# Performance work log

Measured on AMD Instinct MI355X. Metric: run time of the kernel, lower is better.

Reference implementation:

```python
import jax, jax.numpy as jnp
import numpy as np

N = 50000          # num nodes
E = 800000         # num edges
DIN = 128          # in_channels
C = 64             # out_channels per head
H = 2              # heads
ED = 32            # edge_dim


def setup_inputs() -> dict:
    key = jax.random.key(0)
    ks = jax.random.split(key, 12)
    s = 1.0 / np.sqrt(DIN)
    se = 1.0 / np.sqrt(ED)
    return {
        "x": jax.random.normal(ks[0], (N, DIN), dtype=jnp.float32),
        "edge_index": jax.random.randint(ks[1], (2, E), 0, N, dtype=jnp.int32),
        "edge_attr": jax.random.normal(ks[2], (E, ED), dtype=jnp.float32),
        "Wq": jax.random.uniform(ks[3], (DIN, H * C), jnp.float32, -s, s),
        "bq": jax.random.uniform(ks[4], (H * C,), jnp.float32, -s, s),
        "Wk": jax.random.uniform(ks[5], (DIN, H * C), jnp.float32, -s, s),
        "bk": jax.random.uniform(ks[6], (H * C,), jnp.float32, -s, s),
        "Wv": jax.random.uniform(ks[7], (DIN, H * C), jnp.float32, -s, s),
        "bv": jax.random.uniform(ks[8], (H * C,), jnp.float32, -s, s),
        "We": jax.random.uniform(ks[9], (ED, H * C), jnp.float32, -se, se),
        "Wskip": jax.random.uniform(ks[10], (DIN, H * C), jnp.float32, -s, s),
        "bskip": jax.random.uniform(ks[11], (H * C,), jnp.float32, -s, s),
    }


def reference(x, edge_index, edge_attr, Wq, bq, Wk, bk, Wv, bv, We, Wskip, bskip):
    src, dst = edge_index[0], edge_index[1]
    # node-level projections [N, H, C]
    q = (x @ Wq + bq).reshape(N, H, C)
    k = (x @ Wk + bk).reshape(N, H, C)
    v = (x @ Wv + bv).reshape(N, H, C)
    e = (edge_attr @ We).reshape(E, H, C)  # lin_edge, no bias

    # per-edge gather
    q_e = q[dst]              # [E, H, C]
    k_e = k[src] + e          # key gets edge features
    alpha = jnp.einsum("ehc,ehc->eh", q_e, k_e) / jnp.sqrt(jnp.float32(C))

    # segment softmax over incoming edges of each dst node
    m = jax.ops.segment_max(alpha, dst, num_segments=N)       # [N, H]
    alpha = jnp.exp(alpha - m[dst])
    denom = jax.ops.segment_sum(alpha, dst, num_segments=N)   # [N, H]
    alpha = alpha / (denom[dst] + 1e-16)

    # weighted aggregation of values (value also gets edge features)
    msg = (v[src] + e) * alpha[..., None]                     # [E, H, C]
    out = jax.ops.segment_sum(msg, dst, num_segments=N)       # [N, H, C]
    out = out.reshape(N, H * C)

    # root weight skip connection (concat=True, beta=False)
    return out + x @ Wskip + bskip
```

## Files before the change

kernel.cpp:

```cpp
#include <hip/hip_runtime.h>
#include <cstdint>

#define NN 50000
#define EE 800000
#define DINC 128
#define HC 128
#define EDC 32
#define CAP 56
#define TILES 1563
#define SCAT_BLKS 3125
#define NB_SCAN 196
#define PREW_GRID (145 + NB_SCAN)

typedef __attribute__((ext_vector_type(8))) short short8;
typedef __attribute__((ext_vector_type(4))) float floatx4;

__device__ __forceinline__ unsigned int pk2(float a, float b){
  unsigned int ua = __float_as_uint(a), ub = __float_as_uint(b);
  ua = (ua + 0x7FFFu + ((ua >> 16) & 1u)) >> 16;
  ub = (ub + 0x7FFFu + ((ub >> 16) & 1u)) & 0xFFFF0000u;
  return ua | ub;
}
__device__ __forceinline__ float bflo(unsigned int p){ return __uint_as_float(p << 16); }
__device__ __forceinline__ float bfhi(unsigned int p){ return __uint_as_float(p & 0xFFFF0000u); }

__device__ __forceinline__ float red32(float r){
  r += __int_as_float(__builtin_amdgcn_update_dpp(0, __float_as_int(r), 0xB1, 0xF, 0xF, true));
  r += __int_as_float(__builtin_amdgcn_update_dpp(0, __float_as_int(r), 0x4E, 0xF, 0xF, true));
  r += __int_as_float(__builtin_amdgcn_update_dpp(0, __float_as_int(r), 0x141, 0xF, 0xF, true));
  r += __int_as_float(__builtin_amdgcn_update_dpp(0, __float_as_int(r), 0x140, 0xF, 0xF, true));
  r += __shfl_xor(r, 16, 32);
  return r;
}

__global__ __launch_bounds__(256) void k_prew(
    const float* __restrict__ Wq, const float* __restrict__ Wk,
    const float* __restrict__ Wv, const float* __restrict__ Wsk,
    const float* __restrict__ We, const float* __restrict__ bq,
    unsigned int* __restrict__ Wp, unsigned int* __restrict__ Wp5,
    float* __restrict__ Pb, int* __restrict__ cnt)
{
  const int b = blockIdx.x, tid = threadIdx.x;
  if (b < 128){
    int idx = b*256 + tid;
    int mat = idx >> 13;
    int r   = idx & 8191;
    int kp  = r >> 7;
    int n   = r & 127;
    const float* W = (mat==0)?Wq:(mat==1)?Wk:(mat==2)?Wv:Wsk;
    Wp[(mat<<13) + n*64 + kp] = pk2(W[(2*kp)*HC + n], W[(2*kp+1)*HC + n]);
  } else if (b < 144){
    if (!Wp5) return;
    int t = (b-128)*256 + tid;
    int kp = t >> 6, n = t & 63;
    int h = n >> 5, j = n & 31;
    const float* wq0 = Wq + (2*kp)*HC + h*64;
    const float* wq1 = wq0 + HC;
    const float* wer = We + j*HC + h*64;
    float d0 = 0.f, d1 = 0.f;
    #pragma unroll 8
    for (int c = 0; c < 64; ++c){
      float w = wer[c];
      d0 += wq0[c]*w; d1 += wq1[c]*w;
    }
    Wp5[n*64 + kp] = pk2(d0, d1);
  } else if (b == 144){
    if (!Wp5 || tid >= 64) return;
    int n = tid, h = n >> 5, j = n & 31;
    const float* wer = We + j*HC + h*64;
    const float* bqh = bq + h*64;
    float s = 0.f;
    #pragma unroll 8
    for (int c = 0; c < 64; ++c) s += bqh[c]*wer[c];
    Pb[n] = s;
  } else {
    int idx = (b-145)*256 + tid;
    if (idx < NN) cnt[idx] = 0;
  }
}

__global__ __launch_bounds__(256) void k_fused(
    const float* __restrict__ x, const unsigned int* __restrict__ Wp,
    const unsigned int* __restrict__ Wp5, const float* __restrict__ Pb,
    const float* __restrict__ bq, const float* __restrict__ bk,
    const float* __restrict__ bv, const float* __restrict__ bsk,
    const int* __restrict__ ei,
    unsigned int* __restrict__ qbf, unsigned int* __restrict__ kvb,
    float* __restrict__ out, float* __restrict__ Pfl,
    int* __restrict__ cnt, int* __restrict__ eidl,
    const int do_scatter)
{
  __shared__ unsigned int sx[32*68];

  if (do_scatter && blockIdx.x >= TILES){
    int e = (blockIdx.x - TILES)*256 + threadIdx.x;
    if (e < EE){
      int d = ei[EE + e];
      int pos = atomicAdd(cnt + d, 1);
      if (pos < CAP) eidl[d*CAP + pos] = e;
    }
    return;
  }

  const int tid = threadIdx.x;
  const int bm  = blockIdx.x * 32;

  for (int idx = tid; idx < 32*32; idx += 256){
    int row = idx >> 5, kq = idx & 31;
    int gr = bm + row;
    unsigned int p0 = 0u, p1 = 0u;
    if (gr < NN){
      float4 v = *(const float4*)(x + (size_t)gr*DINC + 4*kq);
      p0 = pk2(v.x, v.y); p1 = pk2(v.z, v.w);
    }
    sx[row*68 + 2*kq]     = p0;
    sx[row*68 + 2*kq + 1] = p1;
  }
  __syncthreads();

  const int l = tid & 63, wid = tid >> 6;
  const int lm = l & 15, ks = l >> 4;
  const int pe = lm & 1;
  const int n0 = wid * 32;

  short8 a_f[4][2];
  #pragma unroll
  for (int kb = 0; kb < 4; ++kb){
    a_f[kb][0] = *(const short8*)(sx + lm*68      + kb*16 + ks*4);
    a_f[kb][1] = *(const short8*)(sx + (16+lm)*68 + kb*16 + ks*4);
  }

  #pragma unroll
  for (int mat = 0; mat < 4; ++mat){
    const unsigned int* wp = Wp + (mat<<13);
    const float* bi = (mat==0)?bq:(mat==1)?bk:(mat==2)?bv:bsk;

    floatx4 acc[2][2];
    #pragma unroll
    for (int mt=0;mt<2;mt++)
      #pragma unroll
      for (int nt=0;nt<2;nt++) acc[mt][nt] = (floatx4){0.f,0.f,0.f,0.f};

    #pragma unroll
    for (int kb = 0; kb < 4; ++kb){
      short8 b0 = *(const short8*)(wp + (n0+lm)*64    + kb*16 + ks*4);
      short8 b1 = *(const short8*)(wp + (n0+16+lm)*64 + kb*16 + ks*4);
      acc[0][0] = __builtin_amdgcn_mfma_f32_16x16x32_bf16(a_f[kb][0], b0, acc[0][0], 0, 0, 0);
      acc[0][1] = __builtin_amdgcn_mfma_f32_16x16x32_bf16(a_f[kb][0], b1, acc[0][1], 0, 0, 0);
      acc[1][0] = __builtin_amdgcn_mfma_f32_16x16x32_bf16(a_f[kb][1], b0, acc[1][0], 0, 0, 0);
      acc[1][1] = __builtin_amdgcn_mfma_f32_16x16x32_bf16(a_f[kb][1], b1, acc[1][1], 0, 0, 0);
    }

    if (mat < 3){
      #pragma unroll
      for (int nt=0; nt<2; ++nt){
        const int cbase = n0 + nt*16 + (lm & ~1);
        float2 bb = *(const float2*)(bi + cbase);
        const int cp = cbase >> 1;
        #pragma unroll
        for (int mt=0; mt<2; ++mt){
          #pragma unroll
          for (int s=0; s<2; ++s){
            float a_even = acc[mt][nt][2*s];
            float a_odd  = acc[mt][nt][2*s+1];
            float sw_even = __shfl_xor(a_even, 1, 64);
            float sw_odd  = __shfl_xor(a_odd,  1, 64);
            float self = pe ? a_odd  : a_even;
            float part = pe ? sw_odd : sw_even;
            float lo = pe ? part : self;
            float hi = pe ? self : part;
            unsigned int pv = pk2(lo + bb.x, hi + bb.y);
            int gr = bm + mt*16 + ks*4 + 2*s + pe;
            if (gr < NN){
              if (mat == 0)      qbf[gr*64 + cp] = pv;
              else if (mat == 1) kvb[(size_t)gr*128 + cp]      = pv;
              else               kvb[(size_t)gr*128 + 64 + cp] = pv;
            }
          }
        }
      }
    } else {
      #pragma unroll
      for (int nt=0; nt<2; ++nt){
        const int col = n0 + nt*16 + lm;
        float bs = bi[col];
        #pragma unroll
        for (int mt=0; mt<2; ++mt){
          #pragma unroll
          for (int r=0; r<4; ++r){
            int gr = bm + mt*16 + ks*4 + r;
            if (gr < NN) out[(size_t)gr*HC + col] = acc[mt][nt][r] + bs;
          }
        }
      }
    }
  }

  if (Pfl != nullptr){
    const int mt = wid >> 1;
    const int nq = (wid & 1) * 32;
    floatx4 accp[2];
    accp[0] = (floatx4){0.f,0.f,0.f,0.f};
    accp[1] = (floatx4){0.f,0.f,0.f,0.f};
    #pragma unroll
    for (int kb = 0; kb < 4; ++kb){
      short8 b0 = *(const short8*)(Wp5 + (nq+lm)*64    + kb*16 + ks*4);
      short8 b1 = *(const short8*)(Wp5 + (nq+16+lm)*64 + kb*16 + ks*4);
      accp[0] = __builtin_amdgcn_mfma_f32_16x16x32_bf16(a_f[kb][mt], b0, accp[0], 0, 0, 0);
      accp[1] = __builtin_amdgcn_mfma_f32_16x16x32_bf16(a_f[kb][mt], b1, accp[1], 0, 0, 0);
    }
    #pragma unroll
    for (int nt=0; nt<2; ++nt){
      const int col = nq + nt*16 + lm;
      float bs = Pb[col];
      #pragma unroll
      for (int r=0; r<4; ++r){
        int gr = bm + mt*16 + ks*4 + r;
        if (gr < NN) Pfl[(size_t)gr*64 + col] = accp[nt][r] + bs;
      }
    }
  }
}

__global__ __launch_bounds__(256) void k_count(const int* __restrict__ ei,
    int* __restrict__ cnt)
{
  int e = blockIdx.x*256 + threadIdx.x;
  if (e < EE) atomicAdd(cnt + ei[EE + e], 1);
}
__global__ __launch_bounds__(256) void k_blksum(const int* __restrict__ cnt,
    int* __restrict__ bsum)
{
  __shared__ int s[256];
  int t = threadIdx.x, i = blockIdx.x*256 + t;
  s[t] = (i < NN) ? cnt[i] : 0;
  __syncthreads();
  for (int d = 128; d > 0; d >>= 1){
    if (t < d) s[t] += s[t + d];
    __syncthreads();
  }
  if (t == 0) bsum[blockIdx.x] = s[0];
}
__global__ __launch_bounds__(256) void k_bscan(const int* __restrict__ bsum,
    int* __restrict__ bpre)
{
  __shared__ int s[256];
  int t = threadIdx.x;
  int v = (t < NB_SCAN) ? bsum[t] : 0;
  s[t] = v;
  __syncthreads();
  for (int d = 1; d < 256; d <<= 1){
    int u = (t >= d) ? s[t - d] : 0;
    __syncthreads();
    s[t] += u;
    __syncthreads();
  }
  if (t < NB_SCAN) bpre[t] = s[t] - v;
}
__global__ __launch_bounds__(256) void k_scan3(const int* __restrict__ cnt,
    const int* __restrict__ bpre, int* __restrict__ off, int* __restrict__ woff)
{
  __shared__ int s[256];
  int t = threadIdx.x, i = blockIdx.x*256 + t;
  int v = (i < NN) ? cnt[i] : 0;
  s[t] = v;
  __syncthreads();
  for (int d = 1; d < 256; d <<= 1){
    int u = (t >= d) ? s[t - d] : 0;
    __syncthreads();
    s[t] += u;
    __syncthreads();
  }
  if (i < NN){
    int o = bpre[blockIdx.x] + s[t] - v;
    off[i] = o; woff[i] = o;
  }
}
__global__ __launch_bounds__(256) void k_scatter(const int* __restrict__ ei,
    int* __restrict__ woff, int* __restrict__ eidl)
{
  int e = blockIdx.x*256 + threadIdx.x;
  if (e < EE){
    int d = ei[EE + e];
    int pos = atomicAdd(woff + d, 1);
    eidl[pos] = e;
  }
}

template<int HASP>
__global__ __launch_bounds__(256) void k_agg(
    const float* __restrict__ eattr, const float* __restrict__ We,
    const unsigned int* __restrict__ qbf, const unsigned int* __restrict__ kvb,
    const int* __restrict__ ei,
    const int* __restrict__ cnt, const int* __restrict__ off,
    const int* __restrict__ eidl, const int fixed, const float* __restrict__ Pfl,
    float* __restrict__ out)
{
  __shared__ float sWeT[128*33];
  __shared__ float sWea[256];
  const int tid = threadIdx.x;
  for (int idx = tid; idx < EDC*HC; idx += 256){
    int jj = idx >> 7, col = idx & 127;
    sWeT[col*33 + jj] = We[idx];
  }
  __syncthreads();

  const int wid = tid >> 6, l = tid & 63;
  const int node = blockIdx.x*4 + wid;
  const int h = l >> 5, j = l & 31;

  int deg = cnt[node]; if (deg > CAP) deg = CAP;
  const size_t beg = fixed ? (size_t)node*CAP : (size_t)off[node];
  int eidL = 0, srcL = 0;
  if (deg > 0){
    eidL = eidl[beg + ((l < deg) ? l : 0)];
    srcL = ei[eidL];
  }
  const unsigned int eaOff = (unsigned int)eidL * (EDC*4);
  const unsigned int kOff  = (unsigned int)srcL * 512u;
  const unsigned int jB = (unsigned int)j * 4u;
  const unsigned int lB = (unsigned int)l * 4u;
  const char* eac = (const char*)eattr;
  const char* kvc = (const char*)kvb;

  const float SC = 0.18033688f;
  unsigned int qp = qbf[node*64 + l];
  float q0 = bflo(qp)*SC, q1 = bfhi(qp)*SC;
  float Pl;
  if (HASP){
    Pl = Pfl[(size_t)node*64 + l] * SC;
  } else {
    const uint4* qrow4 = (const uint4*)(qbf + node*64 + h*32);
    const float* wt = sWeT + (h*64)*33 + j;
    float s = 0.f;
    #pragma unroll
    for (int c4 = 0; c4 < 8; ++c4){
      uint4 u = qrow4[c4];
      int b = 8*c4;
      s += bflo(u.x)*wt[(b+0)*33] + bfhi(u.x)*wt[(b+1)*33];
      s += bflo(u.y)*wt[(b+2)*33] + bfhi(u.y)*wt[(b+3)*33];
      s += bflo(u.z)*wt[(b+4)*33] + bfhi(u.z)*wt[(b+5)*33];
      s += bflo(u.w)*wt[(b+6)*33] + bfhi(u.w)*wt[(b+7)*33];
    }
    Pl = s*SC;
  }

#define GATHER(base, EA, KK, VV)                                 \
  {                                                              \
    _Pragma("unroll")                                            \
    for (int t = 0; t < 4; ++t){                                 \
      int s = (base) + t;                                        \
      int it = (s < deg) ? s : 0;                                \
      unsigned int eo = (unsigned int)__shfl((int)eaOff, it, 64) + jB; \
      unsigned int ko = (unsigned int)__shfl((int)kOff,  it, 64) + lB; \
      EA[t] = *(const float*)(eac + eo);                         \
      KK[t] = *(const unsigned int*)(kvc + ko);                  \
      VV[t] = *(const unsigned int*)(kvc + ko + 256);            \
    }                                                            \
  }

  float acc0=0.f, acc1=0.f, wea=0.f, den=0.f;
  if (deg > 0){
    float ea0[4], ea1[4], ea2[4];
    unsigned int kk0[4], kk1[4], kk2[4], vv0[4], vv1[4], vv2[4];
    GATHER(0, ea0, kk0, vv0);
    GATHER(4, ea1, kk1, vv1);
    GATHER(8, ea2, kk2, vv2);

    for (int i = 0; i < deg; i += 4){
      float ean[4]; unsigned int kkn[4], vvn[4];
      if (i + 12 < deg){
        GATHER(i+12, ean, kkn, vvn);
      }
      float p[4];
      #pragma unroll
      for (int t = 0; t < 4; ++t)
        p[t] = q0*bflo(kk0[t]) + q1*bfhi(kk0[t]) + Pl*ea0[t];
      #pragma unroll
      for (int t = 0; t < 4; ++t) p[t] = red32(p[t]);
      const int nb = deg - i;
      #pragma unroll
      for (int t = 0; t < 4; ++t){
        float a = __builtin_amdgcn_exp2f(p[t]);
        if (t > 0) a = (t < nb) ? a : 0.f;
        den  += a;
        acc0 += a*bflo(vv0[t]);
        acc1 += a*bfhi(vv0[t]);
        wea  += a*ea0[t];
      }
      #pragma unroll
      for (int t = 0; t < 4; ++t){
        ea0[t] = ea1[t]; kk0[t] = kk1[t]; vv0[t] = vv1[t];
        ea1[t] = ea2[t]; kk1[t] = kk2[t]; vv1[t] = vv2[t];
        ea2[t] = ean[t]; kk2[t] = kkn[t]; vv2[t] = vvn[t];
      }
    }
  }
#undef GATHER

  sWea[tid] = wea;
  __syncthreads();
  float rden = 1.0f/(den + 1e-16f);
  float e0 = 0.f, e1 = 0.f;
  const float* w0 = sWeT + (2*l)*33;
  const float* w1 = sWeT + (2*l+1)*33;
  const float* wv = sWea + wid*64 + h*32;
  #pragma unroll
  for (int jj = 0; jj < 32; jj += 4){
    float4 w4 = *(const float4*)(wv + jj);
    e0 += w4.x*w0[jj]; e1 += w4.x*w1[jj];
    e0 += w4.y*w0[jj+1]; e1 += w4.y*w1[jj+1];
    e0 += w4.z*w0[jj+2]; e1 += w4.z*w1[jj+2];
    e0 += w4.w*w0[jj+3]; e1 += w4.w*w1[jj+3];
  }
  float2 sk = *(const float2*)(out + (size_t)node*HC + 2*l);
  float2 o;
  o.x = sk.x + (acc0 + e0)*rden;
  o.y = sk.y + (acc1 + e1)*rden;
  *(float2*)(out + (size_t)node*HC + 2*l) = o;
}

extern "C" void kernel_launch(void* const* d_in, const int* in_sizes, int n_in,
                              void* d_out, int out_size, void* d_ws, size_t ws_size,
                              hipStream_t stream)
{
  const float* x   = (const float*)d_in[0];
  const int*   ei  = (const int*)d_in[1];
  const float* ea  = (const float*)d_in[2];
  const float* Wq  = (const float*)d_in[3];
  const float* bq  = (const float*)d_in[4];
  const float* Wk  = (const float*)d_in[5];
  const float* bk  = (const float*)d_in[6];
  const float* Wv  = (const float*)d_in[7];
  const float* bv  = (const float*)d_in[8];
  const float* We  = (const float*)d_in[9];
  const float* Wsk = (const float*)d_in[10];
  const float* bsk = (const float*)d_in[11];
  float* out = (float*)d_out;

  char* ws = (char*)d_ws;
  unsigned int* qbf = (unsigned int*)(ws);
  unsigned int* kvb = (unsigned int*)(ws + 12800000);
  int* cnt = (int*)(ws + 38400000);

  if (ws_size >= 62800000ull){
    int* eidl = (int*)(ws + 38600000);
    unsigned int* Wp  = (unsigned int*)(ws + 49800064);
    unsigned int* Wp5 = (unsigned int*)(ws + 49931264);
    float* Pb  = (float*)(ws + 49947648);
    float* Pfl = (float*)(ws + 49948160);
    k_prew<<<PREW_GRID, 256, 0, stream>>>(Wq, Wk, Wv, Wsk, We, bq, Wp, Wp5, Pb, cnt);
    k_fused<<<TILES + SCAT_BLKS, 256, 0, stream>>>(
        x, Wp, Wp5, Pb, bq, bk, bv, bsk, ei, qbf, kvb, out, Pfl, cnt, eidl, 1);
    k_agg<1><<<12500, 256, 0, stream>>>(ea, We, qbf, kvb, ei,
                                        cnt, (const int*)nullptr, eidl, 1, Pfl, out);
  } else if (ws_size >= 50000000ull){
    int* eidl = (int*)(ws + 38600000);
    unsigned int* Wp = (unsigned int*)(ws + 49800064);
    k_prew<<<PREW_GRID, 256, 0, stream>>>(Wq, Wk, Wv, Wsk, We, bq, Wp, nullptr, nullptr, cnt);
    k_fused<<<TILES + SCAT_BLKS, 256, 0, stream>>>(
        x, Wp, nullptr, nullptr, bq, bk, bv, bsk, ei, qbf, kvb, out, nullptr, cnt, eidl, 1);
    k_agg<0><<<12500, 256, 0, stream>>>(ea, We, qbf, kvb, ei,
                                        cnt, (const int*)nullptr, eidl, 1, nullptr, out);
  } else {
    int* off  = (int*)(ws + 38600000);
    int* woff = (int*)(ws + 38800000);
    int* bsum = (int*)(ws + 39000000);
    int* bpre = (int*)(ws + 39001024);
    int* eidl = (int*)(ws + 39002048);
    unsigned int* Wp = (unsigned int*)(ws + 42202112);
    k_prew<<<PREW_GRID, 256, 0, stream>>>(Wq, Wk, Wv, Wsk, We, bq, Wp, nullptr, nullptr, cnt);
    k_fused<<<TILES, 256, 0, stream>>>(
        x, Wp, nullptr, nullptr, bq, bk, bv, bsk, ei, qbf, kvb, out, nullptr, cnt, nullptr, 0);
    k_count  <<<SCAT_BLKS, 256, 0, stream>>>(ei, cnt);
    k_blksum <<<NB_SCAN, 256, 0, stream>>>(cnt, bsum);
    k_bscan  <<<1, 256, 0, stream>>>(bsum, bpre);
    k_scan3  <<<NB_SCAN, 256, 0, stream>>>(cnt, bpre, off, woff);
    k_scatter<<<SCAT_BLKS, 256, 0, stream>>>(ei, woff, eidl);
    k_agg<0><<<12500, 256, 0, stream>>>(ea, We, qbf, kvb, ei,
                                        cnt, off, eidl, 0, nullptr, out);
  }
}
```

Measured before the change: 409.9 us.

## Interleave K/V rows, pad degree counters, shrink edge-list cap, use readlane gathers

The K and V bf16 projections are now stored interleaved per node, so the aggregation gather fetches both with one 8-byte load instead of two 4-byte loads. The edge-slot broadcast now uses readlane instead of shfl. Per-node degree counters are spaced by a stride of 4 ints, presumably to spread atomic contention, and are zeroed by a memset instead of extra blocks in the prep kernel. The fixed per-node edge capacity drops from 56 to 48 to shrink the edge-id table, which risks dropping edges for nodes with very high in-degree.

Result: slower. 424.3 us (+3.5%).

```diff
diff --git a/kernel.cpp b/kernel.cpp
--- a/kernel.cpp
+++ b/kernel.cpp
@@ -6,11 +6,12 @@
 #define DINC 128
 #define HC 128
 #define EDC 32
-#define CAP 56
+#define CAP 48
+#define CSTR 4
 #define TILES 1563
 #define SCAT_BLKS 3125
 #define NB_SCAN 196
-#define PREW_GRID (145 + NB_SCAN)
+#define PREW_GRID 145
 
 typedef __attribute__((ext_vector_type(8))) short short8;
 typedef __attribute__((ext_vector_type(4))) float floatx4;
@@ -38,7 +39,7 @@
     const float* __restrict__ Wv, const float* __restrict__ Wsk,
     const float* __restrict__ We, const float* __restrict__ bq,
     unsigned int* __restrict__ Wp, unsigned int* __restrict__ Wp5,
-    float* __restrict__ Pb, int* __restrict__ cnt)
+    float* __restrict__ Pb)
 {
   const int b = blockIdx.x, tid = threadIdx.x;
   if (b < 128){
@@ -64,7 +65,7 @@
       d0 += wq0[c]*w; d1 += wq1[c]*w;
     }
     Wp5[n*64 + kp] = pk2(d0, d1);
-  } else if (b == 144){
+  } else {
     if (!Wp5 || tid >= 64) return;
     int n = tid, h = n >> 5, j = n & 31;
     const float* wer = We + j*HC + h*64;
@@ -73,9 +74,6 @@
     #pragma unroll 8
     for (int c = 0; c < 64; ++c) s += bqh[c]*wer[c];
     Pb[n] = s;
-  } else {
-    int idx = (b-145)*256 + tid;
-    if (idx < NN) cnt[idx] = 0;
   }
 }
 
@@ -96,7 +94,7 @@
     int e = (blockIdx.x - TILES)*256 + threadIdx.x;
     if (e < EE){
       int d = ei[EE + e];
-      int pos = atomicAdd(cnt + d, 1);
+      int pos = atomicAdd(cnt + d*CSTR, 1);
       if (pos < CAP) eidl[d*CAP + pos] = e;
     }
     return;
@@ -173,8 +171,8 @@
             int gr = bm + mt*16 + ks*4 + 2*s + pe;
             if (gr < NN){
               if (mat == 0)      qbf[gr*64 + cp] = pv;
-              else if (mat == 1) kvb[(size_t)gr*128 + cp]      = pv;
-              else               kvb[(size_t)gr*128 + 64 + cp] = pv;
+              else if (mat == 1) kvb[(size_t)gr*128 + 2*cp]     = pv;
+              else               kvb[(size_t)gr*128 + 2*cp + 1] = pv;
             }
           }
         }
@@ -226,14 +224,14 @@
     int* __restrict__ cnt)
 {
   int e = blockIdx.x*256 + threadIdx.x;
-  if (e < EE) atomicAdd(cnt + ei[EE + e], 1);
+  if (e < EE) atomicAdd(cnt + ei[EE + e]*CSTR, 1);
 }
 __global__ __launch_bounds__(256) void k_blksum(const int* __restrict__ cnt,
     int* __restrict__ bsum)
 {
   __shared__ int s[256];
   int t = threadIdx.x, i = blockIdx.x*256 + t;
-  s[t] = (i < NN) ? cnt[i] : 0;
+  s[t] = (i < NN) ? cnt[i*CSTR] : 0;
   __syncthreads();
   for (int d = 128; d > 0; d >>= 1){
     if (t < d) s[t] += s[t + d];
@@ -262,7 +260,7 @@
 {
   __shared__ int s[256];
   int t = threadIdx.x, i = blockIdx.x*256 + t;
-  int v = (i < NN) ? cnt[i] : 0;
+  int v = (i < NN) ? cnt[i*CSTR] : 0;
   s[t] = v;
   __syncthreads();
   for (int d = 1; d < 256; d <<= 1){
@@ -309,7 +307,7 @@
   const int node = blockIdx.x*4 + wid;
   const int h = l >> 5, j = l & 31;
 
-  int deg = cnt[node]; if (deg > CAP) deg = CAP;
+  int deg = cnt[node*CSTR]; if (deg > CAP) deg = CAP;
   const size_t beg = fixed ? (size_t)node*CAP : (size_t)off[node];
   int eidL = 0, srcL = 0;
   if (deg > 0){
@@ -319,7 +317,7 @@
   const unsigned int eaOff = (unsigned int)eidL * (EDC*4);
   const unsigned int kOff  = (unsigned int)srcL * 512u;
   const unsigned int jB = (unsigned int)j * 4u;
-  const unsigned int lB = (unsigned int)l * 4u;
+  const unsigned int lB8 = (unsigned int)l * 8u;
   const char* eac = (const char*)eattr;
   const char* kvc = (const char*)kvb;
 
@@ -345,37 +343,36 @@
     Pl = s*SC;
   }
 
-#define GATHER(base, EA, KK, VV)                                 \
-  {                                                              \
-    _Pragma("unroll")                                            \
-    for (int t = 0; t < 4; ++t){                                 \
-      int s = (base) + t;                                        \
-      int it = (s < deg) ? s : 0;                                \
-      unsigned int eo = (unsigned int)__shfl((int)eaOff, it, 64) + jB; \
-      unsigned int ko = (unsigned int)__shfl((int)kOff,  it, 64) + lB; \
-      EA[t] = *(const float*)(eac + eo);                         \
-      KK[t] = *(const unsigned int*)(kvc + ko);                  \
-      VV[t] = *(const unsigned int*)(kvc + ko + 256);            \
-    }                                                            \
+#define GATHER(base, EA, KV)                                          \
+  {                                                                   \
+    _Pragma("unroll")                                                 \
+    for (int t = 0; t < 4; ++t){                                      \
+      int s = (base) + t;                                             \
+      int it = (s < deg) ? s : 0;                                     \
+      unsigned int eo = (unsigned int)__builtin_amdgcn_readlane((int)eaOff, it); \
+      unsigned int ko = (unsigned int)__builtin_amdgcn_readlane((int)kOff,  it); \
+      EA[t] = *(const float*)(eac + eo + jB);                         \
+      KV[t] = *(const uint2*)(kvc + ko + lB8);                        \
+    }                                                                 \
   }
 
   float acc0=0.f, acc1=0.f, wea=0.f, den=0.f;
   if (deg > 0){
     float ea0[4], ea1[4], ea2[4];
-    unsigned int kk0[4], kk1[4], kk2[4], vv0[4], vv1[4], vv2[4];
-    GATHER(0, ea0, kk0, vv0);
-    GATHER(4, ea1, kk1, vv1);
-    GATHER(8, ea2, kk2, vv2);
+    uint2 kv0[4], kv1[4], kv2[4];
+    GATHER(0, ea0, kv0);
+    GATHER(4, ea1, kv1);
+    GATHER(8, ea2, kv2);
 
     for (int i = 0; i < deg; i += 4){
-      float ean[4]; unsigned int kkn[4], vvn[4];
+      float ean[4]; uint2 kvn[4];
       if (i + 12 < deg){
-        GATHER(i+12, ean, kkn, vvn);
+        GATHER(i+12, ean, kvn);
       }
       float p[4];
       #pragma unroll
       for (int t = 0; t < 4; ++t)
-        p[t] = q0*bflo(kk0[t]) + q1*bfhi(kk0[t]) + Pl*ea0[t];
+        p[t] = q0*bflo(kv0[t].x) + q1*bfhi(kv0[t].x) + Pl*ea0[t];
       #pragma unroll
       for (int t = 0; t < 4; ++t) p[t] = red32(p[t]);
       const int nb = deg - i;
@@ -384,15 +381,15 @@
         float a = __builtin_amdgcn_exp2f(p[t]);
         if (t > 0) a = (t < nb) ? a : 0.f;
         den  += a;
-        acc0 += a*bflo(vv0[t]);
-        acc1 += a*bfhi(vv0[t]);
+        acc0 += a*bflo(kv0[t].y);
+        acc1 += a*bfhi(kv0[t].y);
         wea  += a*ea0[t];
       }
       #pragma unroll
       for (int t = 0; t < 4; ++t){
-        ea0[t] = ea1[t]; kk0[t] = kk1[t]; vv0[t] = vv1[t];
-        ea1[t] = ea2[t]; kk1[t] = kk2[t]; vv1[t] = vv2[t];
-        ea2[t] = ean[t]; kk2[t] = kkn[t]; vv2[t] = vvn[t];
+        ea0[t] = ea1[t]; kv0[t] = kv1[t];
+        ea1[t] = ea2[t]; kv1[t] = kv2[t];
+        ea2[t] = ean[t]; kv2[t] = kvn[t];
       }
     }
   }
@@ -443,33 +440,35 @@
   unsigned int* kvb = (unsigned int*)(ws + 12800000);
   int* cnt = (int*)(ws + 38400000);
 
+  hipMemsetAsync(cnt, 0, NN*CSTR*sizeof(int), stream);
+
   if (ws_size >= 62800000ull){
-    int* eidl = (int*)(ws + 38600000);
-    unsigned int* Wp  = (unsigned int*)(ws + 49800064);
-    unsigned int* Wp5 = (unsigned int*)(ws + 49931264);
-    float* Pb  = (float*)(ws + 49947648);
-    float* Pfl = (float*)(ws + 49948160);
-    k_prew<<<PREW_GRID, 256, 0, stream>>>(Wq, Wk, Wv, Wsk, We, bq, Wp, Wp5, Pb, cnt);
+    int* eidl = (int*)(ws + 39200000);
+    unsigned int* Wp  = (unsigned int*)(ws + 48800000);
+    unsigned int* Wp5 = (unsigned int*)(ws + 48931072);
+    float* Pb  = (float*)(ws + 48947456);
+    float* Pfl = (float*)(ws + 48947712);
+    k_prew<<<PREW_GRID, 256, 0, stream>>>(Wq, Wk, Wv, Wsk, We, bq, Wp, Wp5, Pb);
     k_fused<<<TILES + SCAT_BLKS, 256, 0, stream>>>(
         x, Wp, Wp5, Pb, bq, bk, bv, bsk, ei, qbf, kvb, out, Pfl, cnt, eidl, 1);
     k_agg<1><<<12500, 256, 0, stream>>>(ea, We, qbf, kvb, ei,
                                         cnt, (const int*)nullptr, eidl, 1, Pfl, out);
   } else if (ws_size >= 50000000ull){
-    int* eidl = (int*)(ws + 38600000);
-    unsigned int* Wp = (unsigned int*)(ws + 49800064);
-    k_prew<<<PREW_GRID, 256, 0, stream>>>(Wq, Wk, Wv, Wsk, We, bq, Wp, nullptr, nullptr, cnt);
+    int* eidl = (int*)(ws + 39200000);
+    unsigned int* Wp = (unsigned int*)(ws + 48800000);
+    k_prew<<<PREW_GRID, 256, 0, stream>>>(Wq, Wk, Wv, Wsk, We, bq, Wp, nullptr, nullptr);
     k_fused<<<TILES + SCAT_BLKS, 256, 0, stream>>>(
         x, Wp, nullptr, nullptr, bq, bk, bv, bsk, ei, qbf, kvb, out, nullptr, cnt, eidl, 1);
     k_agg<0><<<12500, 256, 0, stream>>>(ea, We, qbf, kvb, ei,
                                         cnt, (const int*)nullptr, eidl, 1, nullptr, out);
   } else {
-    int* off  = (int*)(ws + 38600000);
-    int* woff = (int*)(ws + 38800000);
-    int* bsum = (int*)(ws + 39000000);
-    int* bpre = (int*)(ws + 39001024);
-    int* eidl = (int*)(ws + 39002048);
-    unsigned int* Wp = (unsigned int*)(ws + 42202112);
-    k_prew<<<PREW_GRID, 256, 0, stream>>>(Wq, Wk, Wv, Wsk, We, bq, Wp, nullptr, nullptr, cnt);
+    int* off  = (int*)(ws + 39200000);
+    int* woff = (int*)(ws + 39400000);
+    int* bsum = (int*)(ws + 39600000);
+    int* bpre = (int*)(ws + 39601024);
+    int* eidl = (int*)(ws + 39602048);
+    unsigned int* Wp = (unsigned int*)(ws + 42802048);
+    k_prew<<<PREW_GRID, 256, 0, stream>>>(Wq, Wk, Wv, Wsk, We, bq, Wp, nullptr, nullptr);
     k_fused<<<TILES, 256, 0, stream>>>(
         x, Wp, nullptr, nullptr, bq, bk, bv, bsk, ei, qbf, kvb, out, nullptr, cnt, nullptr, 0);
     k_count  <<<SCAT_BLKS, 256, 0, stream>>>(ei, cnt);
```
